# Optimization experiments

Hardware: AMD Instinct MI355X
Metric: run time of the kernel (lower is better)

## Reference

```python
import jax, jax.numpy as jnp
import numpy as np

B, T = 256, 512
V, H, L, O = 29275, 128, 2, 3


def setup_inputs() -> dict:
    key = jax.random.key(0)
    ks = jax.random.split(key, 8)
    s_emb = 1.0  # torch nn.Embedding default init is N(0,1)
    s = 1.0 / np.sqrt(H)  # torch GRU/Linear default U(-1/sqrt(H), 1/sqrt(H))
    return {
        "x": jax.random.randint(ks[0], (B, T), 0, V, dtype=jnp.int32),
        "emb": jax.random.normal(ks[1], (V, H), dtype=jnp.float32) * s_emb,
        "W_ih": jax.random.uniform(ks[2], (L, 3 * H, H), jnp.float32, -s, s),
        "W_hh": jax.random.uniform(ks[3], (L, 3 * H, H), jnp.float32, -s, s),
        "b_ih": jax.random.uniform(ks[4], (L, 3 * H), jnp.float32, -s, s),
        "b_hh": jax.random.uniform(ks[5], (L, 3 * H), jnp.float32, -s, s),
        "fc_w": jax.random.uniform(ks[6], (O, H), jnp.float32, -s, s),
        "fc_b": jax.random.uniform(ks[7], (O,), jnp.float32, -s, s),
    }


def _gru_layer(inp, Wih, Whh, bih, bhh):
    # inp: [B, T, H]. PyTorch GRU gate order: r, z, n.
    gx = jnp.einsum("bth,gh->btg", inp, Wih) + bih  # [B, T, 3H] input-side gates

    def step(h, gx_t):
        gh = h @ Whh.T + bhh  # [B, 3H]
        xr, xz, xn = jnp.split(gx_t, 3, axis=-1)
        hr, hz, hn = jnp.split(gh, 3, axis=-1)
        r = jax.nn.sigmoid(xr + hr)
        z = jax.nn.sigmoid(xz + hz)
        n = jnp.tanh(xn + r * hn)
        h_new = (1.0 - z) * n + z * h
        return h_new, h_new

    h0 = jnp.zeros((inp.shape[0], Whh.shape[1]), dtype=inp.dtype)
    _, outs = jax.lax.scan(step, h0, gx.transpose(1, 0, 2))  # [T, B, H]
    return outs.transpose(1, 0, 2)


def reference(x, emb, W_ih, W_hh, b_ih, b_hh, fc_w, fc_b):
    h = emb[x]  # [B, T, H] embedding lookup
    for l in range(L):  # small fixed layer count; dropout inactive in eval mode
        h = _gru_layer(h, W_ih[l], W_hh[l], b_ih[l], b_hh[l])
    last = jax.nn.relu(h[:, -1])  # [B, H]
    return last @ fc_w.T + fc_b  # [B, O]
```

## Files before the change

kernel.cpp:

```cpp
#include <hip/hip_runtime.h>
#include <hip/hip_bf16.h>

#define B_   256
#define T_   512
#define H_   128
#define G3_  384

#define TM   128
#define TN   128
#define TK   32
#define LDA  132

#define LOG2E_F  1.4426950408889634f
#define LOG2E2_F 2.8853900817779268f

typedef float v4f __attribute__((ext_vector_type(4)));
typedef float v2f __attribute__((ext_vector_type(2)));

__device__ __forceinline__ float fast_rcp(float x) {
    return __builtin_amdgcn_rcpf(x);
}
__device__ __forceinline__ float exp2_raw(float x) {
    return __builtin_amdgcn_exp2f(x);
}

__device__ __forceinline__ void pk_fma(v2f& acc, v2f a, v2f b) {
    asm("v_pk_fma_f32 %0, %1, %2, %0" : "+v"(acc) : "v"(a), "v"(b));
}

__device__ __forceinline__ float bfly_fold4(float v) {
    int x;
    x = __builtin_amdgcn_update_dpp(0, __float_as_int(v), 0x0B1, 0xF, 0xF, true);
    v += __int_as_float(x);
    x = __builtin_amdgcn_update_dpp(0, __float_as_int(v), 0x04E, 0xF, 0xF, true);
    v += __int_as_float(x);
    return v;
}

__device__ __forceinline__ void lds_barrier() {
    asm volatile("s_waitcnt lgkmcnt(0)" ::: "memory");
    __builtin_amdgcn_s_barrier();
    asm volatile("" ::: "memory");
}

template<bool GATHER>
__global__ __launch_bounds__(256, 2)
void gx_gemm(const float* __restrict__ X,
             const int*   __restrict__ idx,
             const float* __restrict__ emb,
             const float* __restrict__ W,
             const float* __restrict__ bias,
             const float* __restrict__ bias2,
             float*       __restrict__ gx)
{
    __shared__ __align__(16) float As[2][TK][LDA];
    __shared__ __align__(16) float Bs[2][TK][LDA];

    const int tid = threadIdx.x;
    const int tn  = tid & 15;
    const int tm  = tid >> 4;
    const int n0  = blockIdx.x * TN;
    const int m0  = blockIdx.y * TM;

    const int q  = tid & 7;
    const float* rowA[4];
    const float* rowB[4];
#pragma unroll
    for (int s = 0; s < 4; s++) {
        const int r = (tid >> 3) + 32 * s;
        rowA[s] = GATHER ? (emb + (size_t)idx[m0 + r] * H_)
                         : (X + (size_t)(m0 + r) * H_);
        rowB[s] = W + (size_t)(n0 + r) * H_;
    }

    float4 stA[4], stB[4];
    auto load_chunk = [&](int kc) {
#pragma unroll
        for (int s = 0; s < 4; s++) {
            stA[s] = *(const float4*)(rowA[s] + kc + q * 4);
            stB[s] = *(const float4*)(rowB[s] + kc + q * 4);
        }
    };
    auto store_chunk = [&](int buf) {
#pragma unroll
        for (int s = 0; s < 4; s++) {
            const int r = (tid >> 3) + 32 * s;
#pragma unroll
            for (int d = 0; d < 4; d++) {
                As[buf][q * 4 + d][r] = ((const float*)&stA[s])[d];
                Bs[buf][q * 4 + d][r] = ((const float*)&stB[s])[d];
            }
        }
    };

    float4 acc[2][2][4];
#pragma unroll
    for (int a = 0; a < 2; a++)
#pragma unroll
        for (int b = 0; b < 2; b++)
#pragma unroll
            for (int c = 0; c < 4; c++) acc[a][b][c] = make_float4(0.f, 0.f, 0.f, 0.f);

    load_chunk(0);
    store_chunk(0);
    __syncthreads();

    for (int c = 0; c < 4; c++) {
        if (c < 3) load_chunk((c + 1) * TK);
        const int buf = c & 1;
#pragma unroll 4
        for (int k = 0; k < TK; k++) {
            float4 a0 = *(const float4*)&As[buf][k][tm * 4];
            float4 a1 = *(const float4*)&As[buf][k][64 + tm * 4];
            float4 b0 = *(const float4*)&Bs[buf][k][tn * 4];
            float4 b1 = *(const float4*)&Bs[buf][k][64 + tn * 4];
            float4 av[2] = {a0, a1}, bv[2] = {b0, b1};
#pragma unroll
            for (int mg = 0; mg < 2; mg++)
#pragma unroll
                for (int mi = 0; mi < 4; mi++) {
                    const float am = ((const float*)&av[mg])[mi];
#pragma unroll
                    for (int ng = 0; ng < 2; ng++) {
                        acc[mg][ng][mi].x = fmaf(am, bv[ng].x, acc[mg][ng][mi].x);
                        acc[mg][ng][mi].y = fmaf(am, bv[ng].y, acc[mg][ng][mi].y);
                        acc[mg][ng][mi].z = fmaf(am, bv[ng].z, acc[mg][ng][mi].z);
                        acc[mg][ng][mi].w = fmaf(am, bv[ng].w, acc[mg][ng][mi].w);
                    }
                }
        }
        if (c < 3) {
            store_chunk(buf ^ 1);
            __syncthreads();
        }
    }

    float4 bb0 = *(const float4*)(bias + n0 + tn * 4);
    float4 bb1 = *(const float4*)(bias + n0 + 64 + tn * 4);
    if (n0 < 2 * H_) {
        const float4 c0 = *(const float4*)(bias2 + n0 + tn * 4);
        const float4 c1 = *(const float4*)(bias2 + n0 + 64 + tn * 4);
        bb0.x += c0.x; bb0.y += c0.y; bb0.z += c0.z; bb0.w += c0.w;
        bb1.x += c1.x; bb1.y += c1.y; bb1.z += c1.z; bb1.w += c1.w;
    }
    const float esc = (n0 < 2 * H_) ? LOG2E_F : LOG2E2_F;
#pragma unroll
    for (int mg = 0; mg < 2; mg++)
#pragma unroll
        for (int mi = 0; mi < 4; mi++) {
            const int m = m0 + mg * 64 + tm * 4 + mi;
            float* dst = gx + (size_t)m * G3_ + n0;
            float4 v0 = acc[mg][0][mi];
            v0.x = (v0.x + bb0.x) * esc; v0.y = (v0.y + bb0.y) * esc;
            v0.z = (v0.z + bb0.z) * esc; v0.w = (v0.w + bb0.w) * esc;
            float4 v1 = acc[mg][1][mi];
            v1.x = (v1.x + bb1.x) * esc; v1.y = (v1.y + bb1.y) * esc;
            v1.z = (v1.z + bb1.z) * esc; v1.w = (v1.w + bb1.w) * esc;
            *(float4*)(dst + tn * 4) = v0;
            *(float4*)(dst + 64 + tn * 4) = v1;
        }
}

template<bool STORE_H, bool FINAL>
__global__ __launch_bounds__(512)
__attribute__((amdgpu_waves_per_eu(2, 2)))
void gru_recC(const float* __restrict__ gx,
              const float* __restrict__ Whh,
              const float* __restrict__ bhh,
              float*       __restrict__ hseq,
              const float* __restrict__ fc_w,
              const float* __restrict__ fc_b,
              float*       __restrict__ out)
{
    __shared__ __align__(16) float h2[2][H_];

    const int tid = threadIdx.x;
    const int b   = blockIdx.x;
    const int jg  = tid >> 2;
    const int ks  = tid & 3;

    v2f Wr[16], Wz[16], Wn[16];
    {
        const v4f* wr = (const v4f*)(Whh + (size_t)(jg      ) * H_ + ks * 32);
        const v4f* wz = (const v4f*)(Whh + (size_t)(jg + 128) * H_ + ks * 32);
        const v4f* wn = (const v4f*)(Whh + (size_t)(jg + 256) * H_ + ks * 32);
#pragma unroll
        for (int c = 0; c < 8; c++) {
            v4f t;
            t = wr[c] * LOG2E_F;  Wr[2 * c] = t.lo; Wr[2 * c + 1] = t.hi;
            t = wz[c] * LOG2E_F;  Wz[2 * c] = t.lo; Wz[2 * c + 1] = t.hi;
            t = wn[c] * LOG2E2_F; Wn[2 * c] = t.lo; Wn[2 * c + 1] = t.hi;
        }
    }

    const float bhn = bhh[jg + 2 * H_] * LOG2E2_F;

    const float* gxb = gx + (size_t)b * T_ * G3_;
    float gr = gxb[jg], gz = gxb[jg + 128], gn = gxb[jg + 256];
    float h_old = 0.0f;

    if (tid < H_) h2[0][tid] = 0.0f;

    const int hw = ((jg >> 2) & 7) * 16 + (jg >> 5) * 4 + (jg & 3);
    const int hb = ks * 4;

    const float* gnx = gxb + G3_;
    float* hp = STORE_H ? (hseq + (size_t)b * T_ * H_ + jg) : nullptr;

    __syncthreads();

#define GRU_STEPC(HIN, HOUT)                                                  \
    {                                                                         \
        const float gr2_ = gnx[jg];                                           \
        const float gz2_ = gnx[jg + 128];                                     \
        const float gn2_ = gnx[jg + 256];                                     \
        gnx += G3_;                                                           \
        v2f pr = {0.f, 0.f}, pz = {0.f, 0.f}, pn = {0.f, 0.f};                \
        _Pragma("unroll")                                                     \
        for (int c = 0; c < 8; c++) {                                         \
            v4f hv = *(const v4f*)&(HIN)[16 * c + hb];                        \
            v2f hlo = hv.lo, hhi = hv.hi;                                     \
            pk_fma(pr, hlo, Wr[2 * c]);  pk_fma(pr, hhi, Wr[2 * c + 1]);      \
            pk_fma(pz, hlo, Wz[2 * c]);  pk_fma(pz, hhi, Wz[2 * c + 1]);      \
            pk_fma(pn, hlo, Wn[2 * c]);  pk_fma(pn, hhi, Wn[2 * c + 1]);      \
        }                                                                     \
        const float p0 = bfly_fold4(pr.x + pr.y);                             \
        const float p1 = bfly_fold4(pz.x + pz.y);                             \
        const float p2 = bfly_fold4(pn.x + pn.y);                             \
        const float r_ = fast_rcp(1.0f + exp2_raw(-(gr + p0)));               \
        const float z_ = fast_rcp(1.0f + exp2_raw(-(gz + p1)));               \
        const float n_ = fmaf(-2.0f,                                          \
            fast_rcp(exp2_raw(gn + r_ * (p2 + bhn)) + 1.0f), 1.0f);           \
        h_old = fmaf(z_, h_old - n_, n_);                                     \
        if (ks == 0) {                                                        \
            (HOUT)[hw] = h_old;                                               \
            if (STORE_H) *hp = h_old;                                         \
        }                                                                     \
        if (STORE_H) hp += H_;                                                \
        gr = gr2_; gz = gz2_; gn = gn2_;                                      \
        lds_barrier();                                                        \
    }

    for (int t = 0; t < T_; t += 2) {
        GRU_STEPC(h2[0], h2[1])
        GRU_STEPC(h2[1], h2[0])
    }
#undef GRU_STEPC

    if (FINAL) {
        if (ks == 0) h2[1][jg] = fmaxf(h_old, 0.0f);
        __syncthreads();
        if (tid < 3) {
            float acc = fc_b[tid];
            const float* fw = fc_w + tid * H_;
#pragma unroll
            for (int k = 0; k < H_; k++) acc = fmaf(h2[1][k], fw[k], acc);
            out[b * 3 + tid] = acc;
        }
    }
}

template<bool STORE_H, bool FINAL>
__global__ __launch_bounds__(512)
__attribute__((amdgpu_waves_per_eu(2, 2)))
void gru_rec(const float* __restrict__ gx,
             const float* __restrict__ Whh,
             const float* __restrict__ bhh,
             float*       __restrict__ hseq,
             const float* __restrict__ fc_w,
             const float* __restrict__ fc_b,
             float*       __restrict__ out)
{
    __shared__ __align__(16) float h2[2][H_];

    const int tid = threadIdx.x;
    const int b   = blockIdx.x;
    const int jg  = tid >> 2;
    const int ks  = tid & 3;

    v2f Wr[16], Wz[16], Wn[16];
    {
        const v4f* wr = (const v4f*)(Whh + (size_t)(jg      ) * H_ + ks * 32);
        const v4f* wz = (const v4f*)(Whh + (size_t)(jg + 128) * H_ + ks * 32);
        const v4f* wn = (const v4f*)(Whh + (size_t)(jg + 256) * H_ + ks * 32);
#pragma unroll
        for (int c = 0; c < 8; c++) {
            v4f t;
            t = wr[c] * LOG2E_F;  Wr[2 * c] = t.lo; Wr[2 * c + 1] = t.hi;
            t = wz[c] * LOG2E_F;  Wz[2 * c] = t.lo; Wz[2 * c + 1] = t.hi;
            t = wn[c] * LOG2E2_F; Wn[2 * c] = t.lo; Wn[2 * c + 1] = t.hi;
        }
    }

    const float bhn = bhh[jg + 2 * H_] * LOG2E2_F;

    const float* gxb = gx + (size_t)b * T_ * G3_;
    float gr = gxb[jg], gz = gxb[jg + 128], gn = gxb[jg + 256];
    float h_old = 0.0f;

    if (tid < H_) h2[0][tid] = 0.0f;

    const int hw = ((jg >> 2) & 7) * 16 + (jg >> 5) * 4 + (jg & 3);
    const int hb = ks * 4;

    const float* gnx = gxb + G3_;
    float* hp = STORE_H ? (hseq + (size_t)b * T_ * H_ + jg) : nullptr;

    __syncthreads();

#define GRU_STEP(HIN, HOUT)                                                   \
    {                                                                         \
        const float gr2_ = gnx[jg];                                           \
        const float gz2_ = gnx[jg + 128];                                     \
        const float gn2_ = gnx[jg + 256];                                     \
        gnx += G3_;                                                           \
        v2f pr = {0.f, 0.f}, pz = {0.f, 0.f}, pn = {0.f, 0.f};                \
        _Pragma("unroll")                                                     \
        for (int c = 0; c < 8; c++) {                                         \
            v4f hv = *(const v4f*)&(HIN)[16 * c + hb];                        \
            v2f hlo = hv.lo, hhi = hv.hi;                                     \
            pk_fma(pr, hlo, Wr[2 * c]);  pk_fma(pr, hhi, Wr[2 * c + 1]);      \
            pk_fma(pz, hlo, Wz[2 * c]);  pk_fma(pz, hhi, Wz[2 * c + 1]);      \
            pk_fma(pn, hlo, Wn[2 * c]);  pk_fma(pn, hhi, Wn[2 * c + 1]);      \
        }                                                                     \
        const float p0 = bfly_fold4(pr.x + pr.y);                             \
        const float p1 = bfly_fold4(pz.x + pz.y);                             \
        const float p2 = bfly_fold4(pn.x + pn.y);                             \
        const float r_ = fast_rcp(1.0f + exp2_raw(-(gr + p0)));               \
        const float z_ = fast_rcp(1.0f + exp2_raw(-(gz + p1)));               \
        const float n_ = fmaf(-2.0f,                                          \
            fast_rcp(exp2_raw(gn + r_ * (p2 + bhn)) + 1.0f), 1.0f);           \
        h_old = fmaf(z_, h_old - n_, n_);                                     \
        if (ks == 0) {                                                        \
            (HOUT)[hw] = h_old;                                               \
            if (STORE_H) *hp = h_old;                                         \
        }                                                                     \
        if (STORE_H) hp += H_;                                                \
        gr = gr2_; gz = gz2_; gn = gn2_;                                      \
        __syncthreads();                                                      \
    }

    for (int t = 0; t < T_; t += 2) {
        GRU_STEP(h2[0], h2[1])
        GRU_STEP(h2[1], h2[0])
    }
#undef GRU_STEP

    if (FINAL) {
        if (ks == 0) h2[1][jg] = fmaxf(h_old, 0.0f);
        __syncthreads();
        if (tid < 3) {
            float acc = fc_b[tid];
            const float* fw = fc_w + tid * H_;
#pragma unroll
            for (int k = 0; k < H_; k++) acc = fmaf(h2[1][k], fw[k], acc);
            out[b * 3 + tid] = acc;
        }
    }
}

extern "C" void kernel_launch(void* const* d_in, const int* in_sizes, int n_in,
                              void* d_out, int out_size, void* d_ws, size_t ws_size,
                              hipStream_t stream)
{
    const int*   x    = (const int*)  d_in[0];
    const float* emb  = (const float*)d_in[1];
    const float* W_ih = (const float*)d_in[2];
    const float* W_hh = (const float*)d_in[3];
    const float* b_ih = (const float*)d_in[4];
    const float* b_hh = (const float*)d_in[5];
    const float* fc_w = (const float*)d_in[6];
    const float* fc_b = (const float*)d_in[7];
    float* out = (float*)d_out;

    const int M = B_ * T_;
    const size_t gx_f32 = (size_t)M * G3_ * sizeof(float);

    float* gx = (float*)d_ws;
    float* h1 = (float*)((char*)d_ws + gx_f32);

    dim3 ggx(G3_ / TN, M / TM);
    dim3 bgx(256);
    dim3 grec(B_), brec(512);

    hipLaunchKernelGGL((gx_gemm<true>), ggx, bgx, 0, stream,
                       nullptr, x, emb, W_ih, b_ih, b_hh, gx);
    hipLaunchKernelGGL((gru_recC<true, false>), grec, brec, 0, stream,
                       gx, W_hh, b_hh, h1, nullptr, nullptr, nullptr);
    hipLaunchKernelGGL((gx_gemm<false>), ggx, bgx, 0, stream,
                       h1, nullptr, nullptr, W_ih + G3_ * H_, b_ih + G3_,
                       b_hh + G3_, gx);
    hipLaunchKernelGGL((gru_rec<false, true>), grec, brec, 0, stream,
                       gx, W_hh + G3_ * H_, b_hh + G3_, nullptr, fc_w, fc_b, out);
}
```

Before: 929.1 us.

## Fuse layer-2 input projection into layer-1 recurrence, drop intermediate GEMM

The layer-1 recurrence kernel now also holds the layer-2 input weights in registers and computes the layer-2 input-side gate preactivations from each new hidden state. It writes them in place into the gx buffer, at the row for the step just consumed, using the three idle ks lanes. This removes the h1 store, the second gx_gemm launch and its global traffic. In exchange it doubles the weight registers and FMAs per step on the serial critical path, which may lengthen each recurrence step.

Result: faster. 843.3 us (-9.2%).

```diff
diff --git a/kernel.cpp b/kernel.cpp
--- a/kernel.cpp
+++ b/kernel.cpp
@@ -161,16 +161,138 @@
         }
 }
 
+__global__ __launch_bounds__(512)
+__attribute__((amdgpu_waves_per_eu(2, 2)))
+void gru_fused(float*       __restrict__ gx,
+               const float* __restrict__ Whh,
+               const float* __restrict__ bhh,
+               const float* __restrict__ Wih2,
+               const float* __restrict__ bih2,
+               const float* __restrict__ bhh2)
+{
+    __shared__ __align__(16) float h2[2][H_];
+
+    const int tid = threadIdx.x;
+    const int b   = blockIdx.x;
+    const int jg  = tid >> 2;
+    const int ks  = tid & 3;
+
+    v2f Wr[16], Wz[16], Wn[16];
+    v2f Ar[16], Az[16], An[16];
+    {
+        const v4f* wr = (const v4f*)(Whh + (size_t)(jg      ) * H_ + ks * 32);
+        const v4f* wz = (const v4f*)(Whh + (size_t)(jg + 128) * H_ + ks * 32);
+        const v4f* wn = (const v4f*)(Whh + (size_t)(jg + 256) * H_ + ks * 32);
+        const v4f* ar = (const v4f*)(Wih2 + (size_t)(jg      ) * H_ + ks * 32);
+        const v4f* az = (const v4f*)(Wih2 + (size_t)(jg + 128) * H_ + ks * 32);
+        const v4f* an = (const v4f*)(Wih2 + (size_t)(jg + 256) * H_ + ks * 32);
+#pragma unroll
+        for (int c = 0; c < 8; c++) {
+            v4f t;
+            t = wr[c] * LOG2E_F;  Wr[2 * c] = t.lo; Wr[2 * c + 1] = t.hi;
+            t = wz[c] * LOG2E_F;  Wz[2 * c] = t.lo; Wz[2 * c + 1] = t.hi;
+            t = wn[c] * LOG2E2_F; Wn[2 * c] = t.lo; Wn[2 * c + 1] = t.hi;
+            t = ar[c] * LOG2E_F;  Ar[2 * c] = t.lo; Ar[2 * c + 1] = t.hi;
+            t = az[c] * LOG2E_F;  Az[2 * c] = t.lo; Az[2 * c + 1] = t.hi;
+            t = an[c] * LOG2E2_F; An[2 * c] = t.lo; An[2 * c + 1] = t.hi;
+        }
+    }
+
+    const float bhn = bhh[jg + 2 * H_] * LOG2E2_F;
+    const float br2 = (bih2[jg]           + bhh2[jg])           * LOG2E_F;
+    const float bz2 = (bih2[jg + H_]      + bhh2[jg + H_])      * LOG2E_F;
+    const float bn2 =  bih2[jg + 2 * H_]                        * LOG2E2_F;
+
+    float* gxb = gx + (size_t)b * T_ * G3_;
+    float gr = gxb[jg], gz = gxb[jg + 128], gn = gxb[jg + 256];
+    float h_old = 0.0f;
+
+    if (tid < H_) h2[0][tid] = 0.0f;
+
+    const int hw = ((jg >> 2) & 7) * 16 + (jg >> 5) * 4 + (jg & 3);
+    const int hb = ks * 4;
+    const int woff = jg + (ks - 1) * H_;
+
+    const float* gnx = gxb + G3_;
+    float* gxw = gxb - G3_;
+
+    __syncthreads();
+
+#define GRU_STEPF(HIN, HOUT, TT)                                              \
+    {                                                                         \
+        const float gr2_ = gnx[jg];                                           \
+        const float gz2_ = gnx[jg + 128];                                     \
+        const float gn2_ = gnx[jg + 256];                                     \
+        gnx += G3_;                                                           \
+        v2f pr = {0.f, 0.f}, pz = {0.f, 0.f}, pn = {0.f, 0.f};                \
+        v2f qr = {0.f, 0.f}, qz = {0.f, 0.f}, qn = {0.f, 0.f};                \
+        _Pragma("unroll")                                                     \
+        for (int c = 0; c < 8; c++) {                                         \
+            v4f hv = *(const v4f*)&(HIN)[16 * c + hb];                        \
+            v2f hlo = hv.lo, hhi = hv.hi;                                     \
+            pk_fma(pr, hlo, Wr[2 * c]);  pk_fma(pr, hhi, Wr[2 * c + 1]);      \
+            pk_fma(pz, hlo, Wz[2 * c]);  pk_fma(pz, hhi, Wz[2 * c + 1]);      \
+            pk_fma(pn, hlo, Wn[2 * c]);  pk_fma(pn, hhi, Wn[2 * c + 1]);      \
+            pk_fma(qr, hlo, Ar[2 * c]);  pk_fma(qr, hhi, Ar[2 * c + 1]);      \
+            pk_fma(qz, hlo, Az[2 * c]);  pk_fma(qz, hhi, Az[2 * c + 1]);      \
+            pk_fma(qn, hlo, An[2 * c]);  pk_fma(qn, hhi, An[2 * c + 1]);      \
+        }                                                                     \
+        const float p0 = bfly_fold4(pr.x + pr.y);                             \
+        const float p1 = bfly_fold4(pz.x + pz.y);                             \
+        const float p2 = bfly_fold4(pn.x + pn.y);                             \
+        const float q0 = bfly_fold4(qr.x + qr.y) + br2;                       \
+        const float q1 = bfly_fold4(qz.x + qz.y) + bz2;                       \
+        const float q2 = bfly_fold4(qn.x + qn.y) + bn2;                       \
+          \
+        if ((TT) > 0 && ks != 0) {                                            \
+            gxw[woff] = (ks == 1) ? q0 : ((ks == 2) ? q1 : q2);               \
+        }                                                                     \
+        gxw += G3_;                                                           \
+        const float r_ = fast_rcp(1.0f + exp2_raw(-(gr + p0)));               \
+        const float z_ = fast_rcp(1.0f + exp2_raw(-(gz + p1)));               \
+        const float n_ = fmaf(-2.0f,                                          \
+            fast_rcp(exp2_raw(gn + r_ * (p2 + bhn)) + 1.0f), 1.0f);           \
+        h_old = fmaf(z_, h_old - n_, n_);                                     \
+        if (ks == 0) (HOUT)[hw] = h_old;                                      \
+        gr = gr2_; gz = gz2_; gn = gn2_;                                      \
+        lds_barrier();                                                        \
+    }
+
+    for (int t = 0; t < T_; t += 2) {
+        GRU_STEPF(h2[0], h2[1], t)
+        GRU_STEPF(h2[1], h2[0], t + 1)
+    }
+#undef GRU_STEPF
+
+    {
+        v2f qr = {0.f, 0.f}, qz = {0.f, 0.f}, qn = {0.f, 0.f};
+#pragma unroll
+        for (int c = 0; c < 8; c++) {
+            v4f hv = *(const v4f*)&h2[0][16 * c + hb];
+            v2f hlo = hv.lo, hhi = hv.hi;
+            pk_fma(qr, hlo, Ar[2 * c]);  pk_fma(qr, hhi, Ar[2 * c + 1]);
+            pk_fma(qz, hlo, Az[2 * c]);  pk_fma(qz, hhi, Az[2 * c + 1]);
+            pk_fma(qn, hlo, An[2 * c]);  pk_fma(qn, hhi, An[2 * c + 1]);
+        }
+        const float q0 = bfly_fold4(qr.x + qr.y) + br2;
+        const float q1 = bfly_fold4(qz.x + qz.y) + bz2;
+        const float q2 = bfly_fold4(qn.x + qn.y) + bn2;
+        if (ks != 0) {
+            gxw[woff] = (ks == 1) ? q0 : ((ks == 2) ? q1 : q2);
+        }
+    }
+}
+
 template<bool STORE_H, bool FINAL>
 __global__ __launch_bounds__(512)
 __attribute__((amdgpu_waves_per_eu(2, 2)))
-void gru_recC(const float* __restrict__ gx,
-              const float* __restrict__ Whh,
-              const float* __restrict__ bhh,
-              float*       __restrict__ hseq,
-              const float* __restrict__ fc_w,
-              const float* __restrict__ fc_b,
-              float*       __restrict__ out)
+void gru_rec(const float* __restrict__ gx,
+             const float* __restrict__ Whh,
+             const float* __restrict__ bhh,
+             float*       __restrict__ hseq,
+             const float* __restrict__ fc_w,
+             const float* __restrict__ fc_b,
+             float*       __restrict__ out)
 {
     __shared__ __align__(16) float h2[2][H_];
 
@@ -209,7 +331,7 @@
 
     __syncthreads();
 
-#define GRU_STEPC(HIN, HOUT)                                                  \
+#define GRU_STEP(HIN, HOUT)                                                   \
     {                                                                         \
         const float gr2_ = gnx[jg];                                           \
         const float gz2_ = gnx[jg + 128];                                     \
@@ -242,105 +364,6 @@
     }
 
     for (int t = 0; t < T_; t += 2) {
-        GRU_STEPC(h2[0], h2[1])
-        GRU_STEPC(h2[1], h2[0])
-    }
-#undef GRU_STEPC
-
-    if (FINAL) {
-        if (ks == 0) h2[1][jg] = fmaxf(h_old, 0.0f);
-        __syncthreads();
-        if (tid < 3) {
-            float acc = fc_b[tid];
-            const float* fw = fc_w + tid * H_;
-#pragma unroll
-            for (int k = 0; k < H_; k++) acc = fmaf(h2[1][k], fw[k], acc);
-            out[b * 3 + tid] = acc;
-        }
-    }
-}
-
-template<bool STORE_H, bool FINAL>
-__global__ __launch_bounds__(512)
-__attribute__((amdgpu_waves_per_eu(2, 2)))
-void gru_rec(const float* __restrict__ gx,
-             const float* __restrict__ Whh,
-             const float* __restrict__ bhh,
-             float*       __restrict__ hseq,
-             const float* __restrict__ fc_w,
-             const float* __restrict__ fc_b,
-             float*       __restrict__ out)
-{
-    __shared__ __align__(16) float h2[2][H_];
-
-    const int tid = threadIdx.x;
-    const int b   = blockIdx.x;
-    const int jg  = tid >> 2;
-    const int ks  = tid & 3;
-
-    v2f Wr[16], Wz[16], Wn[16];
-    {
-        const v4f* wr = (const v4f*)(Whh + (size_t)(jg      ) * H_ + ks * 32);
-        const v4f* wz = (const v4f*)(Whh + (size_t)(jg + 128) * H_ + ks * 32);
-        const v4f* wn = (const v4f*)(Whh + (size_t)(jg + 256) * H_ + ks * 32);
-#pragma unroll
-        for (int c = 0; c < 8; c++) {
-            v4f t;
-            t = wr[c] * LOG2E_F;  Wr[2 * c] = t.lo; Wr[2 * c + 1] = t.hi;
-            t = wz[c] * LOG2E_F;  Wz[2 * c] = t.lo; Wz[2 * c + 1] = t.hi;
-            t = wn[c] * LOG2E2_F; Wn[2 * c] = t.lo; Wn[2 * c + 1] = t.hi;
-        }
-    }
-
-    const float bhn = bhh[jg + 2 * H_] * LOG2E2_F;
-
-    const float* gxb = gx + (size_t)b * T_ * G3_;
-    float gr = gxb[jg], gz = gxb[jg + 128], gn = gxb[jg + 256];
-    float h_old = 0.0f;
-
-    if (tid < H_) h2[0][tid] = 0.0f;
-
-    const int hw = ((jg >> 2) & 7) * 16 + (jg >> 5) * 4 + (jg & 3);
-    const int hb = ks * 4;
-
-    const float* gnx = gxb + G3_;
-    float* hp = STORE_H ? (hseq + (size_t)b * T_ * H_ + jg) : nullptr;
-
-    __syncthreads();
-
-#define GRU_STEP(HIN, HOUT)                                                   \
-    {                                                                         \
-        const float gr2_ = gnx[jg];                                           \
-        const float gz2_ = gnx[jg + 128];                                     \
-        const float gn2_ = gnx[jg + 256];                                     \
-        gnx += G3_;                                                           \
-        v2f pr = {0.f, 0.f}, pz = {0.f, 0.f}, pn = {0.f, 0.f};                \
-        _Pragma("unroll")                                                     \
-        for (int c = 0; c < 8; c++) {                                         \
-            v4f hv = *(const v4f*)&(HIN)[16 * c + hb];                        \
-            v2f hlo = hv.lo, hhi = hv.hi;                                     \
-            pk_fma(pr, hlo, Wr[2 * c]);  pk_fma(pr, hhi, Wr[2 * c + 1]);      \
-            pk_fma(pz, hlo, Wz[2 * c]);  pk_fma(pz, hhi, Wz[2 * c + 1]);      \
-            pk_fma(pn, hlo, Wn[2 * c]);  pk_fma(pn, hhi, Wn[2 * c + 1]);      \
-        }                                                                     \
-        const float p0 = bfly_fold4(pr.x + pr.y);                             \
-        const float p1 = bfly_fold4(pz.x + pz.y);                             \
-        const float p2 = bfly_fold4(pn.x + pn.y);                             \
-        const float r_ = fast_rcp(1.0f + exp2_raw(-(gr + p0)));               \
-        const float z_ = fast_rcp(1.0f + exp2_raw(-(gz + p1)));               \
-        const float n_ = fmaf(-2.0f,                                          \
-            fast_rcp(exp2_raw(gn + r_ * (p2 + bhn)) + 1.0f), 1.0f);           \
-        h_old = fmaf(z_, h_old - n_, n_);                                     \
-        if (ks == 0) {                                                        \
-            (HOUT)[hw] = h_old;                                               \
-            if (STORE_H) *hp = h_old;                                         \
-        }                                                                     \
-        if (STORE_H) hp += H_;                                                \
-        gr = gr2_; gz = gz2_; gn = gn2_;                                      \
-        __syncthreads();                                                      \
-    }
-
-    for (int t = 0; t < T_; t += 2) {
         GRU_STEP(h2[0], h2[1])
         GRU_STEP(h2[1], h2[0])
     }
@@ -374,10 +397,8 @@
     float* out = (float*)d_out;
 
     const int M = B_ * T_;
-    const size_t gx_f32 = (size_t)M * G3_ * sizeof(float);
 
     float* gx = (float*)d_ws;
-    float* h1 = (float*)((char*)d_ws + gx_f32);
 
     dim3 ggx(G3_ / TN, M / TM);
     dim3 bgx(256);
@@ -385,11 +406,9 @@
 
     hipLaunchKernelGGL((gx_gemm<true>), ggx, bgx, 0, stream,
                        nullptr, x, emb, W_ih, b_ih, b_hh, gx);
-    hipLaunchKernelGGL((gru_recC<true, false>), grec, brec, 0, stream,
-                       gx, W_hh, b_hh, h1, nullptr, nullptr, nullptr);
-    hipLaunchKernelGGL((gx_gemm<false>), ggx, bgx, 0, stream,
-                       h1, nullptr, nullptr, W_ih + G3_ * H_, b_ih + G3_,
-                       b_hh + G3_, gx);
+    hipLaunchKernelGGL(gru_fused, grec, brec, 0, stream,
+                       gx, W_hh, b_hh,
+                       W_ih + G3_ * H_, b_ih + G3_, b_hh + G3_);
     hipLaunchKernelGGL((gru_rec<false, true>), grec, brec, 0, stream,
                        gx, W_hh + G3_ * H_, b_hh + G3_, nullptr, fc_w, fc_b, out);
 }
```
